# Kernel tuning notes

Measured on AMD Instinct MI355X. Metric: run time of the kernel, lower is better.

The kernel has to match this reference:

```python
import jax, jax.numpy as jnp
import numpy as np

H, W = 512, 512          # image_shape
FH, FW = 64, 64          # filter_size
NUM_PARTS = 256
N = 8192                 # number of placed parts


def setup_inputs() -> dict:
    key = jax.random.key(0)
    k1, k2, k3, k4 = jax.random.split(key, 4)
    filters = jax.random.normal(k1, (NUM_PARTS, FH, FW), dtype=jnp.float32)
    part = jax.random.randint(k2, (N,), 0, NUM_PARTS)
    row = jax.random.randint(k3, (N,), 0, H)
    col = jax.random.randint(k4, (N,), 0, W)
    phw_list = jnp.stack([part, row, col], axis=1).astype(jnp.int32)  # [N,3]
    return {"phw_list": phw_list, "filters": filters}


def reference(phw_list, filters):
    # Original: for each part i, slice filters[part_idx] to the in-bounds window
    # and += into canvas[from_r:to_r, from_c:to_c].
    # Equivalent vectorized form: scatter-add FULL filters onto a padded canvas
    # (pad = full filter size on each side, so all writes are in-bounds), then
    # crop back to (H, W). Clipping via crop == the original's slice clipping.
    fo_h, fo_w = FH // 2, FW // 2  # filter center offsets
    part = phw_list[:, 0]
    row = phw_list[:, 1]
    col = phw_list[:, 2]

    filts = filters[part]                                  # (N, FH, FW) gather
    r0 = row - fo_h + FH                                   # top-left row in padded canvas
    c0 = col - fo_w + FW                                   # top-left col in padded canvas
    rr = r0[:, None, None] + jnp.arange(FH)[None, :, None]  # (N, FH, 1)
    cc = c0[:, None, None] + jnp.arange(FW)[None, None, :]  # (N, 1, FW)

    padded = jnp.zeros((H + 2 * FH, W + 2 * FW), dtype=filters.dtype)
    padded = padded.at[rr, cc].add(filts)                  # overlapping scatter-add
    return padded[FH:FH + H, FW:FW + W]                    # (H, W) canvas
```

## Files before the change

### kernel.cpp

```cpp
#include <hip/hip_runtime.h>


#define H_  512
#define W_  512
#define FH_ 64
#define FW_ 64
#define TILE_ 32
#define THREADS_ 256
#define SEG_LEN_ 1024

__device__ __forceinline__ int clamp63(int v) {
    return min(max(v, 0), 63);
}

__global__ __launch_bounds__(THREADS_, 8)
void render_tile_kernel(const int* __restrict__ phw,
                        const float* __restrict__ filters,
                        float* __restrict__ out, int n) {
    __shared__ unsigned int s_list[SEG_LEN_];
    __shared__ int s_cnt;

    const int t   = threadIdx.x;
    const int tx0 = blockIdx.x * TILE_;
    const int ty0 = blockIdx.y * TILE_;
    const int k0  = blockIdx.z * SEG_LEN_;
    const int k1  = (k0 + SEG_LEN_ < n) ? (k0 + SEG_LEN_) : n;

    if (t == 0) s_cnt = 0;
    __syncthreads();

    for (int k = k0 + t; k < k1; k += THREADS_) {
        const int part = phw[k * 3 + 0];
        const int row  = phw[k * 3 + 1];
        const int col  = phw[k * 3 + 2];
        const bool hit =
            (row >= ty0 - (FH_ / 2 - 1)) && (row <= ty0 + TILE_ - 1 + FH_ / 2) &&
            (col >= tx0 - (FW_ / 2 - 1)) && (col <= tx0 + TILE_ - 1 + FW_ / 2);
        if (hit) {
            const int idx = atomicAdd(&s_cnt, 1);
            s_list[idx] = ((unsigned)part << 18) | ((unsigned)row << 9) | (unsigned)col;
        }
    }
    __syncthreads();
    const int cnt = s_cnt;

    const int xl    = t & 31;
    const int yb    = t >> 5;
    const int x     = tx0 + xl;
    const int ybase = ty0 + yb;

    float acc0 = 0.f, acc1 = 0.f, acc2 = 0.f, acc3 = 0.f;

    auto body = [&](unsigned v) {
        const int part = (int)__builtin_amdgcn_readfirstlane(v >> 18);
        const int row  = (int)__builtin_amdgcn_readfirstlane((v >> 9) & 511u);
        const int col  = (int)__builtin_amdgcn_readfirstlane(v & 511u);
        const float* __restrict__ f = filters + (part << 12);

        const int  j   = x - col + (FW_ / 2);
        const int  jc  = clamp63(j);
        const bool jok = (unsigned)j < (unsigned)FW_;
        const int  i0  = ybase - row + (FH_ / 2);

        const int ia = i0;      const int ib = i0 + 8;
        const int ic = i0 + 16; const int id = i0 + 24;
        const float va = f[clamp63(ia) * FW_ + jc];
        const float vb = f[clamp63(ib) * FW_ + jc];
        const float vc = f[clamp63(ic) * FW_ + jc];
        const float vd = f[clamp63(id) * FW_ + jc];
        acc0 += (jok && (unsigned)ia < (unsigned)FH_) ? va : 0.f;
        acc1 += (jok && (unsigned)ib < (unsigned)FH_) ? vb : 0.f;
        acc2 += (jok && (unsigned)ic < (unsigned)FH_) ? vc : 0.f;
        acc3 += (jok && (unsigned)id < (unsigned)FH_) ? vd : 0.f;
    };

    int k = 0;
    for (; k + 4 <= cnt; k += 4) {
        const uint4 vv = *(const uint4*)&s_list[k];
        body(vv.x); body(vv.y); body(vv.z); body(vv.w);
    }
    for (; k < cnt; ++k) body(s_list[k]);

    atomicAdd(&out[(ybase +  0) * W_ + x], acc0);
    atomicAdd(&out[(ybase +  8) * W_ + x], acc1);
    atomicAdd(&out[(ybase + 16) * W_ + x], acc2);
    atomicAdd(&out[(ybase + 24) * W_ + x], acc3);
}

extern "C" void kernel_launch(void* const* d_in, const int* in_sizes, int n_in,
                              void* d_out, int out_size, void* d_ws, size_t ws_size,
                              hipStream_t stream) {
    const int*   phw     = (const int*)d_in[0];
    const float* filters = (const float*)d_in[1];
    float*       out     = (float*)d_out;
    const int n = in_sizes[0] / 3;

    hipMemsetAsync(out, 0, (size_t)H_ * W_ * sizeof(float), stream);

    const int segs = (n + SEG_LEN_ - 1) / SEG_LEN_;
    dim3 grid(W_ / TILE_, H_ / TILE_, segs);
    render_tile_kernel<<<grid, THREADS_, 0, stream>>>(phw, filters, out, n);
}
```

Baseline: 81.70 us.

## Zero-pad filters into workspace to drop bounds checks and vectorize loads

A pre-pass copies each 64x64 filter into the center of a zero-padded 128x128 buffer in workspace, and the same kernel also zeroes the output in place of the memset. The render kernel then maps each thread to 4 consecutive columns and reads a single unaligned 16-byte vector per placed part, with no clamping or masking, because out-of-window reads land in the zero padding. This removes the per-element bounds arithmetic and cuts four scalar loads to one vector load. In exchange it needs 16 MB of padded filters, which raises cache footprint, and it adds an extra kernel launch.

```diff
diff --git a/kernel.cpp b/kernel.cpp
--- a/kernel.cpp
+++ b/kernel.cpp
@@ -5,17 +5,40 @@
 #define W_  512
 #define FH_ 64
 #define FW_ 64
+#define NPARTS_ 256
+#define PFH_ 128
+#define PFW_ 128
 #define TILE_ 32
 #define THREADS_ 256
 #define SEG_LEN_ 1024
 
-__device__ __forceinline__ int clamp63(int v) {
-    return min(max(v, 0), 63);
+struct __attribute__((packed, aligned(4))) f4u { float x, y, z, w; };
+
+__global__ __launch_bounds__(256)
+void pad_filters_kernel(const float* __restrict__ filters,
+                        float* __restrict__ fpad,
+                        float* __restrict__ out) {
+    const int part = blockIdx.x;
+    const int t    = threadIdx.x;
+    float4* dst = (float4*)(fpad + part * (PFH_ * PFW_));
+    const float* src = filters + part * (FH_ * FW_);
+#pragma unroll
+    for (int it = 0; it < 16; ++it) {
+        const int slot = t + 256 * it;
+        const int pr   = slot >> 5;
+        const int pc4  = (slot & 31) * 4;
+        float4 v = make_float4(0.f, 0.f, 0.f, 0.f);
+        if (pr >= 32 && pr < 96 && pc4 >= 32 && pc4 < 96) {
+            v = *(const float4*)(src + (pr - 32) * FW_ + (pc4 - 32));
+        }
+        dst[slot] = v;
+    }
+    ((float4*)out)[part * 256 + t] = make_float4(0.f, 0.f, 0.f, 0.f);
 }
 
 __global__ __launch_bounds__(THREADS_, 8)
 void render_tile_kernel(const int* __restrict__ phw,
-                        const float* __restrict__ filters,
+                        const float* __restrict__ fpad,
                         float* __restrict__ out, int n) {
     __shared__ unsigned int s_list[SEG_LEN_];
     __shared__ int s_cnt;
@@ -44,10 +67,9 @@
     __syncthreads();
     const int cnt = s_cnt;
 
-    const int xl    = t & 31;
-    const int yb    = t >> 5;
-    const int x     = tx0 + xl;
-    const int ybase = ty0 + yb;
+    const int x0 = tx0 + (t & 7) * 4;
+    const int y  = ty0 + (t >> 3);
+    const int voff = y * PFW_ + x0;
 
     float acc0 = 0.f, acc1 = 0.f, acc2 = 0.f, acc3 = 0.f;
 
@@ -55,23 +77,10 @@
         const int part = (int)__builtin_amdgcn_readfirstlane(v >> 18);
         const int row  = (int)__builtin_amdgcn_readfirstlane((v >> 9) & 511u);
         const int col  = (int)__builtin_amdgcn_readfirstlane(v & 511u);
-        const float* __restrict__ f = filters + (part << 12);
-
-        const int  j   = x - col + (FW_ / 2);
-        const int  jc  = clamp63(j);
-        const bool jok = (unsigned)j < (unsigned)FW_;
-        const int  i0  = ybase - row + (FH_ / 2);
-
-        const int ia = i0;      const int ib = i0 + 8;
-        const int ic = i0 + 16; const int id = i0 + 24;
-        const float va = f[clamp63(ia) * FW_ + jc];
-        const float vb = f[clamp63(ib) * FW_ + jc];
-        const float vc = f[clamp63(ic) * FW_ + jc];
-        const float vd = f[clamp63(id) * FW_ + jc];
-        acc0 += (jok && (unsigned)ia < (unsigned)FH_) ? va : 0.f;
-        acc1 += (jok && (unsigned)ib < (unsigned)FH_) ? vb : 0.f;
-        acc2 += (jok && (unsigned)ic < (unsigned)FH_) ? vc : 0.f;
-        acc3 += (jok && (unsigned)id < (unsigned)FH_) ? vd : 0.f;
+        const float* __restrict__ f =
+            fpad + part * (PFH_ * PFW_) + ((64 - row) * PFW_ + (64 - col));
+        const f4u w = *(const f4u*)(f + voff);
+        acc0 += w.x; acc1 += w.y; acc2 += w.z; acc3 += w.w;
     };
 
     int k = 0;
@@ -81,10 +90,11 @@
     }
     for (; k < cnt; ++k) body(s_list[k]);
 
-    atomicAdd(&out[(ybase +  0) * W_ + x], acc0);
-    atomicAdd(&out[(ybase +  8) * W_ + x], acc1);
-    atomicAdd(&out[(ybase + 16) * W_ + x], acc2);
-    atomicAdd(&out[(ybase + 24) * W_ + x], acc3);
+    float* o = out + y * W_ + x0;
+    atomicAdd(o + 0, acc0);
+    atomicAdd(o + 1, acc1);
+    atomicAdd(o + 2, acc2);
+    atomicAdd(o + 3, acc3);
 }
 
 extern "C" void kernel_launch(void* const* d_in, const int* in_sizes, int n_in,
@@ -93,11 +103,12 @@
     const int*   phw     = (const int*)d_in[0];
     const float* filters = (const float*)d_in[1];
     float*       out     = (float*)d_out;
+    float*       fpad    = (float*)d_ws;
     const int n = in_sizes[0] / 3;
 
-    hipMemsetAsync(out, 0, (size_t)H_ * W_ * sizeof(float), stream);
+    pad_filters_kernel<<<NPARTS_, 256, 0, stream>>>(filters, fpad, out);
 
     const int segs = (n + SEG_LEN_ - 1) / SEG_LEN_;
     dim3 grid(W_ / TILE_, H_ / TILE_, segs);
-    render_tile_kernel<<<grid, THREADS_, 0, stream>>>(phw, filters, out, n);
+    render_tile_kernel<<<grid, THREADS_, 0, stream>>>(phw, fpad, out, n);
 }
```

New measurement: 126.4 us. +54.7%, slower.
